# Kernel optimization log

Hardware: AMD Instinct MI355X
Metric: run time of the kernel (lower is better)

## Reference

```python
import jax, jax.numpy as jnp
import numpy as np

B, N, C, H, K = 8, 1024, 768, 12, 16


def setup_inputs() -> dict:
    key = jax.random.key(0)
    ks = jax.random.split(key, 5)
    s = 0.02
    return {
        "query": jax.random.normal(ks[0], (B, N, C), jnp.float32),
        "in_proj_weight": jax.random.normal(ks[1], (3 * C, C), jnp.float32) * s,
        "in_proj_bias": jax.random.normal(ks[2], (3 * C,), jnp.float32) * s,
        "out_proj_weight": jax.random.normal(ks[3], (C, C), jnp.float32) * s,
        "out_proj_bias": jax.random.normal(ks[4], (C,), jnp.float32) * s,
        "num_heads": H,
        "k": K,
    }


def reference(query, in_proj_weight, in_proj_bias, out_proj_weight, out_proj_bias, num_heads, k):
    b, n, c = query.shape
    hd = c // num_heads
    scale = hd ** (-0.5)
    # fused QKV projection: F.linear(x, W, b) == x @ W.T + b
    qkv = query @ in_proj_weight.T + in_proj_bias  # [B,N,3C]
    qkv = qkv.reshape(b, n, 3, num_heads, hd).transpose(2, 0, 3, 1, 4)  # [3,B,H,N,hd]
    q, kk, v = qkv[0], qkv[1], qkv[2]
    attn = jnp.einsum("bhqd,bhkd->bhqk", q, kk) * scale
    attn = jax.nn.softmax(attn, axis=-1)  # [B,H,N,N]
    kk_ = min(k, attn.shape[-1])
    vals, idx = jax.lax.top_k(attn, kk_)  # [B,H,N,k]
    bi = jnp.arange(b)[:, None, None, None]
    hi = jnp.arange(num_heads)[None, :, None, None]
    ni = jnp.arange(n)[None, None, :, None]
    topk_attn = jnp.zeros_like(attn).at[bi, hi, ni, idx].set(vals)
    den = jnp.clip(topk_attn.sum(axis=-1, keepdims=True), 1e-6, None)
    topk_attn = topk_attn / den
    out = jnp.einsum("bhqk,bhkd->bhqd", topk_attn, v)  # [B,H,N,hd]
    out = out.transpose(0, 2, 1, 3).reshape(b, n, c)
    out = out @ out_proj_weight.T + out_proj_bias
    return out, topk_attn
```

## Files before the change

### kernel.cpp

```cpp
#include <hip/hip_runtime.h>
#include <float.h>
#include <math.h>

#define B_ 8
#define N_ 1024
#define C_ 768
#define H_ 12
#define HD_ 64
#define BH_ (B_*H_)

__device__ __forceinline__ unsigned long long makekey(float v, int idx) {
    unsigned int b = __float_as_uint(v);
    unsigned int o = (b & 0x80000000u) ? ~b : (b | 0x80000000u);
    return ((unsigned long long)o << 32) | (unsigned int)(1023 - idx);
}
__device__ __forceinline__ float keyval(unsigned long long k) {
    unsigned int ordv = (unsigned int)(k >> 32);
    unsigned int fb = (ordv & 0x80000000u) ? (ordv & 0x7FFFFFFFu) : ~ordv;
    return __uint_as_float(fb);
}

template<int MM, int NN, int KD, int MODE>
__global__ void __launch_bounds__(256)
gemm_k(const float* __restrict__ A, const float* __restrict__ W,
       const float* __restrict__ bias, float* __restrict__ out)
{
    __shared__ float As[2][16][132];
    __shared__ float Bs[2][16][132];
    const int tid = threadIdx.x;
    constexpr int NBLK = NN / 128;
    constexpr int NWG = (MM / 128) * NBLK;
    const int eff = (blockIdx.x & 7) * (NWG / 8) + (blockIdx.x >> 3);
    const int bm = eff / NBLK;
    const int bn = eff % NBLK;
    const int m0 = bm * 128, n0 = bn * 128;
    const int ty = tid >> 4, tx = tid & 15;
    const int ar = tid >> 2;
    const int ac = (tid & 3) << 2;

    float acc[8][8];
#pragma unroll
    for (int i = 0; i < 8; ++i)
#pragma unroll
        for (int j = 0; j < 8; ++j) acc[i][j] = 0.f;

    const float* A0 = A + (size_t)(m0 + ar) * KD + ac;
    const float* A1 = A + (size_t)(m0 + ar + 64) * KD + ac;
    const float* W0 = W + (size_t)(n0 + ar) * KD + ac;
    const float* W1 = W + (size_t)(n0 + ar + 64) * KD + ac;

    float4 pa0 = *(const float4*)A0;
    float4 pa1 = *(const float4*)A1;
    float4 pb0 = *(const float4*)W0;
    float4 pb1 = *(const float4*)W1;

    As[0][ac+0][ar]    = pa0.x; As[0][ac+1][ar]    = pa0.y; As[0][ac+2][ar]    = pa0.z; As[0][ac+3][ar]    = pa0.w;
    As[0][ac+0][ar+64] = pa1.x; As[0][ac+1][ar+64] = pa1.y; As[0][ac+2][ar+64] = pa1.z; As[0][ac+3][ar+64] = pa1.w;
    Bs[0][ac+0][ar]    = pb0.x; Bs[0][ac+1][ar]    = pb0.y; Bs[0][ac+2][ar]    = pb0.z; Bs[0][ac+3][ar]    = pb0.w;
    Bs[0][ac+0][ar+64] = pb1.x; Bs[0][ac+1][ar+64] = pb1.y; Bs[0][ac+2][ar+64] = pb1.z; Bs[0][ac+3][ar+64] = pb1.w;
    __syncthreads();

    int cur = 0;
    for (int k0 = 0; k0 < KD; k0 += 16) {
        const bool more = (k0 + 16 < KD);
        if (more) {
            pa0 = *(const float4*)(A0 + k0 + 16);
            pa1 = *(const float4*)(A1 + k0 + 16);
            pb0 = *(const float4*)(W0 + k0 + 16);
            pb1 = *(const float4*)(W1 + k0 + 16);
        }
        const float (*Ac)[132] = As[cur];
        const float (*Bc)[132] = Bs[cur];
#pragma unroll
        for (int kk = 0; kk < 16; ++kk) {
            float4 a0v = *(const float4*)&Ac[kk][ty * 4];
            float4 a1v = *(const float4*)&Ac[kk][64 + ty * 4];
            float4 b0v = *(const float4*)&Bc[kk][tx * 4];
            float4 b1v = *(const float4*)&Bc[kk][64 + tx * 4];
            float av[8] = {a0v.x,a0v.y,a0v.z,a0v.w, a1v.x,a1v.y,a1v.z,a1v.w};
            float bv[8] = {b0v.x,b0v.y,b0v.z,b0v.w, b1v.x,b1v.y,b1v.z,b1v.w};
#pragma unroll
            for (int i = 0; i < 8; ++i)
#pragma unroll
                for (int j = 0; j < 8; ++j)
                    acc[i][j] = fmaf(av[i], bv[j], acc[i][j]);
        }
        if (more) {
            const int nxt = cur ^ 1;
            As[nxt][ac+0][ar]    = pa0.x; As[nxt][ac+1][ar]    = pa0.y; As[nxt][ac+2][ar]    = pa0.z; As[nxt][ac+3][ar]    = pa0.w;
            As[nxt][ac+0][ar+64] = pa1.x; As[nxt][ac+1][ar+64] = pa1.y; As[nxt][ac+2][ar+64] = pa1.z; As[nxt][ac+3][ar+64] = pa1.w;
            Bs[nxt][ac+0][ar]    = pb0.x; Bs[nxt][ac+1][ar]    = pb0.y; Bs[nxt][ac+2][ar]    = pb0.z; Bs[nxt][ac+3][ar]    = pb0.w;
            Bs[nxt][ac+0][ar+64] = pb1.x; Bs[nxt][ac+1][ar+64] = pb1.y; Bs[nxt][ac+2][ar+64] = pb1.z; Bs[nxt][ac+3][ar+64] = pb1.w;
            __syncthreads();
            cur = nxt;
        }
    }

#pragma unroll
    for (int gi = 0; gi < 2; ++gi)
#pragma unroll
    for (int i = 0; i < 4; ++i) {
        const int m = m0 + gi * 64 + ty * 4 + i;
        const int ai = gi * 4 + i;
#pragma unroll
        for (int gj = 0; gj < 2; ++gj) {
            const int o = n0 + gj * 64 + tx * 4;
            const int aj = gj * 4;
            float4 bv4 = *(const float4*)(bias + o);
            float4 v;
            v.x = acc[ai][aj+0] + bv4.x;
            v.y = acc[ai][aj+1] + bv4.y;
            v.z = acc[ai][aj+2] + bv4.z;
            v.w = acc[ai][aj+3] + bv4.w;
            if (MODE == 0) {
                *(float4*)(out + (size_t)m * NN + o) = v;
            } else {
                const int which = o / 768;
                const int r = o - which * 768;
                const int hh = r >> 6;
                const int dd = r & 63;
                const int bh = (m >> 10) * H_ + hh;
                const int nn = m & 1023;
                if (which == 1) {
                    float* dst = out + (size_t)BH_ * N_ * HD_
                               + ((size_t)bh * HD_ + dd) * N_ + nn;
                    dst[0]      = v.x;
                    dst[N_]     = v.y;
                    dst[2 * N_] = v.z;
                    dst[3 * N_] = v.w;
                } else {
                    float* dst = out + (size_t)which * ((size_t)BH_ * N_ * HD_)
                               + ((size_t)bh * N_ + nn) * HD_ + dd;
                    *(float4*)dst = v;
                }
            }
        }
    }
}

__global__ void __launch_bounds__(512, 8)
attn_k(const float* __restrict__ Qg, const float* __restrict__ Ktg,
       uint2* __restrict__ wlist)
{
    __shared__ float Qs[64][8];
    __shared__ float qm[8][64];
    __shared__ unsigned long long kbuf[8][384];
    __shared__ int cnt[8][4];
    __shared__ uint2 w16s[8][16];

    const int tid = threadIdx.x;
    const int lane = tid & 63;
    const int w = tid >> 6;
    const int rg = w >> 2;
    const int cg = w & 3;
    const int eff = (blockIdx.x & 7) * 1536 + (blockIdx.x >> 3);
    const int bh = eff >> 7;
    const int qt = eff & 127;
    const int q0 = qt << 3;
    const size_t kvbase = (size_t)bh * (N_ * HD_);

    if (tid < 128) {
        int q = tid >> 4;
        int d4 = (tid & 15) << 2;
        float4 v = *(const float4*)(Qg + kvbase + (size_t)(q0 + q) * HD_ + d4);
        Qs[d4+0][q] = v.x; Qs[d4+1][q] = v.y; Qs[d4+2][q] = v.z; Qs[d4+3][q] = v.w;
    }
    __syncthreads();

    float acc[4][4];
#pragma unroll
    for (int r = 0; r < 4; ++r)
#pragma unroll
        for (int u = 0; u < 4; ++u) acc[r][u] = 0.f;

    const int jb = (cg << 8) + (lane << 2);
    const int r0 = rg << 2;
    const float* kcol = Ktg + kvbase + jb;

#pragma unroll 8
    for (int d = 0; d < 64; ++d) {
        float4 kvv = *(const float4*)(kcol + (d << 10));
        float4 qa = *(const float4*)&Qs[d][r0];
        float qv[4] = {qa.x, qa.y, qa.z, qa.w};
#pragma unroll
        for (int r = 0; r < 4; ++r) {
            acc[r][0] = fmaf(qv[r], kvv.x, acc[r][0]);
            acc[r][1] = fmaf(qv[r], kvv.y, acc[r][1]);
            acc[r][2] = fmaf(qv[r], kvv.z, acc[r][2]);
            acc[r][3] = fmaf(qv[r], kvv.w, acc[r][3]);
        }
    }

#pragma unroll
    for (int r = 0; r < 4; ++r)
#pragma unroll
        for (int u = 0; u < 4; ++u) acc[r][u] *= 0.125f;

#pragma unroll
    for (int rr = 0; rr < 4; ++rr) {
        float lm = fmaxf(fmaxf(acc[rr][0], acc[rr][1]), fmaxf(acc[rr][2], acc[rr][3]));
        lm = fmaxf(lm, __shfl_xor(lm, 1));
        lm = fmaxf(lm, __shfl_xor(lm, 2));
        if ((lane & 3) == 0) qm[r0 + rr][(cg << 4) + (lane >> 2)] = lm;
    }
    __syncthreads();

#pragma unroll
    for (int rr = 0; rr < 4; ++rr) {
        const int r = r0 + rr;
        const int g = lane & 15;
        float sg = fmaxf(fmaxf(qm[r][g], qm[r][16 + g]),
                         fmaxf(qm[r][32 + g], qm[r][48 + g]));
        sg = fminf(sg, __shfl_xor(sg, 1));
        sg = fminf(sg, __shfl_xor(sg, 2));
        sg = fminf(sg, __shfl_xor(sg, 4));
        sg = fminf(sg, __shfl_xor(sg, 8));
        const float T = sg;
        int base = 0;
        unsigned long long lowmask = (lane == 0) ? 0ull : ((1ull << lane) - 1ull);
#pragma unroll
        for (int u = 0; u < 4; ++u) {
            bool f = acc[rr][u] >= T;
            unsigned long long m = __ballot(f);
            int pos = base + __popcll(m & lowmask);
            if (f && pos < 96) kbuf[r][cg * 96 + pos] = makekey(acc[rr][u], jb + u);
            base += __popcll(m);
        }
        if (lane == 0) cnt[r][cg] = base < 96 ? base : 96;
    }
    __syncthreads();

    {
        const int r = w;
        const int c0n = cnt[r][0], c1n = cnt[r][1], c2n = cnt[r][2], c3n = cnt[r][3];
        const int pfx1 = c0n, pfx2 = c0n + c1n, pfx3 = c0n + c1n + c2n;
        const int Ctot = pfx3 + c3n;

        auto mapk = [&](int p) -> unsigned long long {
            if (p >= Ctot) return 0ull;
            int wseg, pos;
            if (p < pfx1)      { wseg = 0; pos = p; }
            else if (p < pfx2) { wseg = 1; pos = p - pfx1; }
            else if (p < pfx3) { wseg = 2; pos = p - pfx2; }
            else               { wseg = 3; pos = p - pfx3; }
            return kbuf[r][wseg * 96 + pos];
        };

        if (Ctot <= 128) {
            unsigned long long kk0 = mapk(lane);
            unsigned long long kk1 = mapk(lane + 64);
            int n0 = 0, n1 = 0;
#pragma unroll 1
            for (int seg = 0; seg < 4; ++seg) {
                const int cn = cnt[r][seg];
                const unsigned long long* sp = &kbuf[r][seg * 96];
#pragma unroll 4
                for (int p = 0; p < cn; ++p) {
                    unsigned long long kp = sp[p];
                    n0 += (kp > kk0); n1 += (kp > kk1);
                }
            }
            float v0 = keyval(kk0), v1 = keyval(kk1);
            float mc = -FLT_MAX;
            if (n0 == 0) mc = v0;
            if (n1 == 0) mc = v1;
#pragma unroll
            for (int off = 1; off < 64; off <<= 1) mc = fmaxf(mc, __shfl_xor(mc, off));
            float e0 = (n0 < 16) ? expf(v0 - mc) : 0.f;
            float e1 = (n1 < 16) ? expf(v1 - mc) : 0.f;
            float es = e0 + e1;
#pragma unroll
            for (int off = 1; off < 64; off <<= 1) es += __shfl_xor(es, off);
            if (n0 < 16) w16s[r][n0] = make_uint2(1023u - (unsigned)(kk0 & 0xFFFFFFFFull), __float_as_uint(e0 / es));
            if (n1 < 16) w16s[r][n1] = make_uint2(1023u - (unsigned)(kk1 & 0xFFFFFFFFull), __float_as_uint(e1 / es));
        } else {
            unsigned long long kk0 = mapk(lane);
            unsigned long long kk1 = mapk(lane + 64);
            unsigned long long kk2 = mapk(lane + 128);
            unsigned long long kk3 = mapk(lane + 192);
            unsigned long long kk4 = mapk(lane + 256);
            unsigned long long kk5 = mapk(lane + 320);
            int n0 = 0, n1 = 0, n2 = 0, n3 = 0, n4 = 0, n5 = 0;
#pragma unroll 1
            for (int seg = 0; seg < 4; ++seg) {
                const int cn = cnt[r][seg];
                const unsigned long long* sp = &kbuf[r][seg * 96];
#pragma unroll 2
                for (int p = 0; p < cn; ++p) {
                    unsigned long long kp = sp[p];
                    n0 += (kp > kk0); n1 += (kp > kk1); n2 += (kp > kk2);
                    n3 += (kp > kk3); n4 += (kp > kk4); n5 += (kp > kk5);
                }
            }
            float v0 = keyval(kk0), v1 = keyval(kk1), v2 = keyval(kk2);
            float v3 = keyval(kk3), v4 = keyval(kk4), v5 = keyval(kk5);
            float mc = -FLT_MAX;
            if (n0 == 0) mc = v0;
            if (n1 == 0) mc = v1;
            if (n2 == 0) mc = v2;
            if (n3 == 0) mc = v3;
            if (n4 == 0) mc = v4;
            if (n5 == 0) mc = v5;
#pragma unroll
            for (int off = 1; off < 64; off <<= 1) mc = fmaxf(mc, __shfl_xor(mc, off));
            float e0 = (n0 < 16) ? expf(v0 - mc) : 0.f;
            float e1 = (n1 < 16) ? expf(v1 - mc) : 0.f;
            float e2 = (n2 < 16) ? expf(v2 - mc) : 0.f;
            float e3 = (n3 < 16) ? expf(v3 - mc) : 0.f;
            float e4 = (n4 < 16) ? expf(v4 - mc) : 0.f;
            float e5 = (n5 < 16) ? expf(v5 - mc) : 0.f;
            float es = e0 + e1 + e2 + e3 + e4 + e5;
#pragma unroll
            for (int off = 1; off < 64; off <<= 1) es += __shfl_xor(es, off);
            if (n0 < 16) w16s[r][n0] = make_uint2(1023u - (unsigned)(kk0 & 0xFFFFFFFFull), __float_as_uint(e0 / es));
            if (n1 < 16) w16s[r][n1] = make_uint2(1023u - (unsigned)(kk1 & 0xFFFFFFFFull), __float_as_uint(e1 / es));
            if (n2 < 16) w16s[r][n2] = make_uint2(1023u - (unsigned)(kk2 & 0xFFFFFFFFull), __float_as_uint(e2 / es));
            if (n3 < 16) w16s[r][n3] = make_uint2(1023u - (unsigned)(kk3 & 0xFFFFFFFFull), __float_as_uint(e3 / es));
            if (n4 < 16) w16s[r][n4] = make_uint2(1023u - (unsigned)(kk4 & 0xFFFFFFFFull), __float_as_uint(e4 / es));
            if (n5 < 16) w16s[r][n5] = make_uint2(1023u - (unsigned)(kk5 & 0xFFFFFFFFull), __float_as_uint(e5 / es));
        }
        asm volatile("s_waitcnt lgkmcnt(0)" ::: "memory");
        __builtin_amdgcn_sched_barrier(0);

        if (lane < 16)
            wlist[((size_t)bh * N_ + q0 + r) * 16 + lane] = w16s[r][lane];
    }
}

__global__ void __launch_bounds__(256)
pv_scatter_k(const uint2* __restrict__ wlist, const float* __restrict__ Vg,
             float* __restrict__ topk, float* __restrict__ aout)
{
    const int tid = threadIdx.x;
    const int lane = tid & 63;
    const int row = (blockIdx.x << 2) + (tid >> 6);
    const size_t base = (size_t)row << 10;
    const int bh = row >> 10;
    const int n = row & 1023;
    const int b = bh / H_;
    const int h = bh - b * H_;

    float4 z4; z4.x = z4.y = z4.z = z4.w = 0.f;
#pragma unroll
    for (int t = 0; t < 4; ++t)
        *(float4*)(topk + base + (size_t)(((t << 6) + lane) << 2)) = z4;

    const uint2* wl = wlist + (size_t)row * 16;
    const float* vb = Vg + (size_t)bh * (N_ * HD_);
    float pacc = 0.f;
#pragma unroll
    for (int t = 0; t < 16; ++t) {
        uint2 e = wl[t];
        pacc = fmaf(__uint_as_float(e.y), vb[((size_t)e.x << 6) + lane], pacc);
    }
    aout[((size_t)(b * N_ + n)) * C_ + (h << 6) + lane] = pacc;

    asm volatile("s_waitcnt vmcnt(0)" ::: "memory");
    if (lane < 16) {
        uint2 e = wl[lane];
        topk[base + e.x] = __uint_as_float(e.y);
    }
}

extern "C" void kernel_launch(void* const* d_in, const int* in_sizes, int n_in,
                              void* d_out, int out_size, void* d_ws, size_t ws_size,
                              hipStream_t stream)
{
    (void)in_sizes; (void)n_in; (void)out_size; (void)ws_size;
    const float* query = (const float*)d_in[0];
    const float* win   = (const float*)d_in[1];
    const float* bin   = (const float*)d_in[2];
    const float* wout  = (const float*)d_in[3];
    const float* bout  = (const float*)d_in[4];

    float* ws = (float*)d_ws;
    float* Qp   = ws;
    float* Ktg  = Qp  + (size_t)BH_ * N_ * HD_;
    float* Vp   = Ktg + (size_t)BH_ * N_ * HD_;
    float* aout = Vp  + (size_t)BH_ * N_ * HD_;
    uint2* wlist = (uint2*)(aout + (size_t)B_ * N_ * C_);

    float* outp = (float*)d_out;
    float* topk = outp + (size_t)B_ * N_ * C_;

    gemm_k<8192, 2304, 768, 1><<<64 * 18, 256, 0, stream>>>(query, win, bin, Qp);
    attn_k<<<BH_ * 128, 512, 0, stream>>>(Qp, Ktg, wlist);
    pv_scatter_k<<<BH_ * N_ / 4, 256, 0, stream>>>(wlist, Vp, topk, aout);
    gemm_k<8192, 768, 768, 0><<<64 * 6, 256, 0, stream>>>(aout, wout, bout, outp);
}
```

Baseline: 939.6 us.

## Use bf16 MFMA GEMM for V projection and output projection

Splits the fused QKV projection so the Q/K part stays on the fp32 SIMT GEMM while V is computed by a new bf16 MFMA GEMM that converts fp32 tiles to bf16 in shared memory. The output projection also switches to the bf16 MFMA kernel. Q/K stay fp32, which keeps the top-k selection exact, and the cheaper precision is used only where the values are consumed linearly. The cost is bf16 rounding error in V and the output. The new kernel has no double buffering and writes its results with scalar stores.

```diff
diff --git a/kernel.cpp b/kernel.cpp
--- a/kernel.cpp
+++ b/kernel.cpp
@@ -9,6 +9,9 @@
 #define HD_ 64
 #define BH_ (B_*H_)
 
+typedef __attribute__((ext_vector_type(8))) short bf16x8;
+typedef __attribute__((ext_vector_type(4))) float f32x4;
+
 __device__ __forceinline__ unsigned long long makekey(float v, int idx) {
     unsigned int b = __float_as_uint(v);
     unsigned int o = (b & 0x80000000u) ? ~b : (b | 0x80000000u);
@@ -18,6 +21,10 @@
     unsigned int ordv = (unsigned int)(k >> 32);
     unsigned int fb = (ordv & 0x80000000u) ? (ordv & 0x7FFFFFFFu) : ~ordv;
     return __uint_as_float(fb);
+}
+__device__ __forceinline__ unsigned short f2bf(float f) {
+    unsigned int u = __float_as_uint(f);
+    return (unsigned short)((u + 0x7FFFu + ((u >> 16) & 1u)) >> 16);
 }
 
 template<int MM, int NN, int KD, int MODE>
@@ -129,9 +136,104 @@
                     dst[2 * N_] = v.z;
                     dst[3 * N_] = v.w;
                 } else {
-                    float* dst = out + (size_t)which * ((size_t)BH_ * N_ * HD_)
-                               + ((size_t)bh * N_ + nn) * HD_ + dd;
+                    float* dst = out + ((size_t)bh * N_ + nn) * HD_ + dd;
                     *(float4*)dst = v;
+                }
+            }
+        }
+    }
+}
+
+template<int MM, int NN, int MODE>
+__global__ void __launch_bounds__(256)
+gemm_bf_k(const float* __restrict__ A, const float* __restrict__ W,
+          const float* __restrict__ bias, float* __restrict__ out)
+{
+    __shared__ unsigned short Asb[128][40];
+    __shared__ unsigned short Bsb[128][40];
+    const int tid = threadIdx.x;
+    constexpr int NBLK = NN / 128;
+    constexpr int NWG = (MM / 128) * NBLK;
+    const int eff = (blockIdx.x & 7) * (NWG / 8) + (blockIdx.x >> 3);
+    const int bm = eff / NBLK;
+    const int bn = eff % NBLK;
+    const int m0 = bm * 128, n0 = bn * 128;
+    const int lane = tid & 63;
+    const int w = tid >> 6;
+    const int wm = (w >> 1) << 6;
+    const int wn = (w & 1) << 6;
+
+    f32x4 acc[4][4];
+#pragma unroll
+    for (int i = 0; i < 4; ++i)
+#pragma unroll
+        for (int j = 0; j < 4; ++j) acc[i][j] = (f32x4){0.f, 0.f, 0.f, 0.f};
+
+    const int srow = tid >> 1;
+    const int sks  = (tid & 1) << 4;
+    const float* ga = A + (size_t)(m0 + srow) * 768 + sks;
+    const float* gw = W + (size_t)(n0 + srow) * 768 + sks;
+
+    for (int k0 = 0; k0 < 768; k0 += 32) {
+        __syncthreads();
+        {
+            float4 f0 = *(const float4*)(ga + k0 + 0);
+            float4 f1 = *(const float4*)(ga + k0 + 4);
+            float4 f2 = *(const float4*)(ga + k0 + 8);
+            float4 f3 = *(const float4*)(ga + k0 + 12);
+            unsigned short* d = &Asb[srow][sks];
+            d[0]=f2bf(f0.x);  d[1]=f2bf(f0.y);  d[2]=f2bf(f0.z);  d[3]=f2bf(f0.w);
+            d[4]=f2bf(f1.x);  d[5]=f2bf(f1.y);  d[6]=f2bf(f1.z);  d[7]=f2bf(f1.w);
+            d[8]=f2bf(f2.x);  d[9]=f2bf(f2.y);  d[10]=f2bf(f2.z); d[11]=f2bf(f2.w);
+            d[12]=f2bf(f3.x); d[13]=f2bf(f3.y); d[14]=f2bf(f3.z); d[15]=f2bf(f3.w);
+            f0 = *(const float4*)(gw + k0 + 0);
+            f1 = *(const float4*)(gw + k0 + 4);
+            f2 = *(const float4*)(gw + k0 + 8);
+            f3 = *(const float4*)(gw + k0 + 12);
+            unsigned short* e = &Bsb[srow][sks];
+            e[0]=f2bf(f0.x);  e[1]=f2bf(f0.y);  e[2]=f2bf(f0.z);  e[3]=f2bf(f0.w);
+            e[4]=f2bf(f1.x);  e[5]=f2bf(f1.y);  e[6]=f2bf(f1.z);  e[7]=f2bf(f1.w);
+            e[8]=f2bf(f2.x);  e[9]=f2bf(f2.y);  e[10]=f2bf(f2.z); e[11]=f2bf(f2.w);
+            e[12]=f2bf(f3.x); e[13]=f2bf(f3.y); e[14]=f2bf(f3.z); e[15]=f2bf(f3.w);
+        }
+        __syncthreads();
+
+        bf16x8 af[4], bf[4];
+        const int fr = lane & 15;
+        const int fk = (lane >> 4) << 3;
+#pragma unroll
+        for (int fi = 0; fi < 4; ++fi)
+            af[fi] = *(const bf16x8*)&Asb[wm + (fi << 4) + fr][fk];
+#pragma unroll
+        for (int fj = 0; fj < 4; ++fj)
+            bf[fj] = *(const bf16x8*)&Bsb[wn + (fj << 4) + fr][fk];
+#pragma unroll
+        for (int fi = 0; fi < 4; ++fi)
+#pragma unroll
+            for (int fj = 0; fj < 4; ++fj)
+                acc[fi][fj] = __builtin_amdgcn_mfma_f32_16x16x32_bf16(af[fi], bf[fj], acc[fi][fj], 0, 0, 0);
+    }
+
+    const int cr = (lane >> 4) << 2;
+    const int cc = lane & 15;
+#pragma unroll
+    for (int fj = 0; fj < 4; ++fj) {
+        const int col = n0 + wn + (fj << 4) + cc;
+        const float bb = bias[col];
+#pragma unroll
+        for (int fi = 0; fi < 4; ++fi) {
+#pragma unroll
+            for (int j = 0; j < 4; ++j) {
+                const int row = m0 + wm + (fi << 4) + cr + j;
+                const float val = acc[fi][fj][j] + bb;
+                if (MODE == 0) {
+                    out[(size_t)row * NN + col] = val;
+                } else {
+                    const int hh = col >> 6;
+                    const int dd = col & 63;
+                    const int bh = (row >> 10) * H_ + hh;
+                    const int nn = row & 1023;
+                    out[((size_t)bh * N_ + nn) * HD_ + dd] = val;
                 }
             }
         }
@@ -383,8 +485,10 @@
     float* outp = (float*)d_out;
     float* topk = outp + (size_t)B_ * N_ * C_;
 
-    gemm_k<8192, 2304, 768, 1><<<64 * 18, 256, 0, stream>>>(query, win, bin, Qp);
+    gemm_k<8192, 1536, 768, 1><<<64 * 12, 256, 0, stream>>>(query, win, bin, Qp);
+    gemm_bf_k<8192, 768, 2><<<64 * 6, 256, 0, stream>>>(query, win + (size_t)1536 * 768,
+                                                        bin + 1536, Vp);
     attn_k<<<BH_ * 128, 512, 0, stream>>>(Qp, Ktg, wlist);
     pv_scatter_k<<<BH_ * N_ / 4, 256, 0, stream>>>(wlist, Vp, topk, aout);
-    gemm_k<8192, 768, 768, 0><<<64 * 6, 256, 0, stream>>>(aout, wout, bout, outp);
-}
+    gemm_bf_k<8192, 768, 0><<<64 * 6, 256, 0, stream>>>(aout, wout, bout, outp);
+}
```

Measured after the change: 772.6 us. 1.22x faster.
